# Performance work log

Hardware: AMD Instinct MI355X
Metric: run time of the kernel (lower is better)

The kernel has to match this reference:

```python
import jax, jax.numpy as jnp
import numpy as np

N = 50000      # nodes
E = 800000     # edges (before self loops)
IN_DIM = 256
HID = 64       # per-head hidden dim
HEADS = 4
NEG_SLOPE = 0.2


def setup_inputs() -> dict:
    key = jax.random.key(0)
    k1, k2, k3, k4, k5, k6 = jax.random.split(key, 6)
    x = jax.random.normal(k1, (N, IN_DIM), dtype=jnp.float32)
    edge_index = jax.random.randint(k2, (2, E), 0, N, dtype=jnp.int64)
    # GATConv params (PyG layout): lin weight, att_src, att_dst, bias
    W = jax.random.normal(k3, (IN_DIM, HEADS * HID), dtype=jnp.float32) / np.sqrt(IN_DIM)
    att_src = jax.random.normal(k4, (HEADS, HID), dtype=jnp.float32) / np.sqrt(HID)
    att_dst = jax.random.normal(k5, (HEADS, HID), dtype=jnp.float32) / np.sqrt(HID)
    bias = jnp.zeros((HEADS * HID,), dtype=jnp.float32)
    return {"x": x, "edge_index": edge_index, "W": W,
            "att_src": att_src, "att_dst": att_dst, "bias": bias}


def _gat_forward(x, edge_index, W, att_src, att_dst, bias):
    n = x.shape[0]
    # linear projection per head: [N, H, F]
    h = (x @ W).reshape(n, HEADS, HID)
    # per-node attention logits (computed once on nodes, then gathered)
    a_src = jnp.einsum('nhf,hf->nh', h, att_src)  # [N, H]
    a_dst = jnp.einsum('nhf,hf->nh', h, att_dst)  # [N, H]
    # add self loops (PyG default add_self_loops=True)
    loop = jnp.arange(n, dtype=edge_index.dtype)
    src = jnp.concatenate([edge_index[0], loop])  # [E+N]
    dst = jnp.concatenate([edge_index[1], loop])  # [E+N]
    # edge attention logits with LeakyReLU
    e = jax.nn.leaky_relu(a_src[src] + a_dst[dst], NEG_SLOPE)  # [E+N, H]
    # segment softmax over incoming edges of each destination node
    m = jax.ops.segment_max(e, dst, num_segments=n)            # [N, H]
    num = jnp.exp(e - m[dst])                                  # [E+N, H]
    denom = jax.ops.segment_sum(num, dst, num_segments=n)      # [N, H]
    alpha = num / denom[dst]                                   # [E+N, H]
    # scatter-aggregate weighted source features
    msg = alpha[:, :, None] * h[src]                           # [E+N, H, F]
    out = jax.ops.segment_sum(msg, dst, num_segments=n)        # [N, H, F]
    out = out.reshape(n, HEADS * HID) + bias
    # GraphEncoder.forward: ReLU then Dropout (dropout=0 -> identity)
    return jax.nn.relu(out)


def reference(x, edge_index, W, att_src, att_dst, bias):
    return _gat_forward(x, edge_index, W, att_src, att_dst, bias)
```

## Files before the change

kernel.cpp:

```cpp
#include <hip/hip_runtime.h>
#include <hip/hip_bf16.h>

#define N_NODES 50000
#define N_EDGES 800000
#define TOT_EDGES (N_EDGES + N_NODES)
#define IN_DIM 256
#define OUT_DIM 256
#define HEADS 4
#define NEG_SLOPE 0.2f
#define CAP 96

#define GBLK 782
#define LDS_STRIDE 264

typedef __bf16 bf16x8 __attribute__((ext_vector_type(8)));
typedef __bf16 bf16x4 __attribute__((ext_vector_type(4)));
typedef float f32x4 __attribute__((ext_vector_type(4)));

__device__ __forceinline__ float b2f(unsigned short u) {
    union { float f; unsigned int i; } v; v.i = ((unsigned int)u) << 16; return v.f;
}

__device__ __forceinline__ bool detect64(const int* __restrict__ ei, int t) {
    int nz = 0;
    for (int i = t; i < 1024; i += 256)
        if (ei[2 * i + 1] != 0) nz++;
    return __syncthreads_count(nz) == 0;
}

struct Args {
    const float* x; const int* ei; const float* W;
    const float* att_s; const float* att_d; const float* bias;
    float* out;
    __bf16* Wt; __bf16* h; float* a_src; float* a_dst;
    int* counts; int* ell;
};

__global__ void k_wt(Args A) {
    int k = blockIdx.x;
    int n = threadIdx.x;
    A.Wt[(size_t)n * IN_DIM + k] = (__bf16)A.W[(size_t)k * OUT_DIM + n];
}

__global__ __launch_bounds__(256) void k_fill(Args A) {
    bool is64 = detect64(A.ei, threadIdx.x);
    int i = blockIdx.x * 256 + threadIdx.x;
    const long long* ei64 = (const long long*)A.ei;
    if (i < N_EDGES) {
        int s, d;
        if (is64) { s = (int)ei64[i]; d = (int)ei64[N_EDGES + i]; }
        else      { s = A.ei[i];      d = A.ei[N_EDGES + i]; }
        int pos = atomicAdd(&A.counts[d], 1);
        if (pos < CAP) A.ell[(size_t)d * CAP + pos] = s;
    } else if (i < TOT_EDGES) {
        int n = i - N_EDGES;
        int pos = atomicAdd(&A.counts[n], 1);
        if (pos < CAP) A.ell[(size_t)n * CAP + pos] = n;
    }
}

__global__ __launch_bounds__(256) void k_gemm(Args A) {
    __shared__ __bf16 xs[64 * LDS_STRIDE];
    const int t = threadIdx.x;
    const int mbase = blockIdx.x * 64;
    const float4* __restrict__ x4 = (const float4*)A.x;
    const __bf16* __restrict__ Wt = A.Wt;

#pragma unroll
    for (int i = 0; i < 16; ++i) {
        int f = i * 256 + t;
        int row = f >> 6;
        int c4  = f & 63;
        int grow = mbase + row;
        if (grow >= N_NODES) grow = N_NODES - 1;
        float4 v = x4[(size_t)grow * 64 + c4];
        bf16x4 o = { (__bf16)v.x, (__bf16)v.y, (__bf16)v.z, (__bf16)v.w };
        *(bf16x4*)&xs[row * LDS_STRIDE + c4 * 4] = o;
    }
    __syncthreads();

    const int wave = t >> 6;
    const int lane = t & 63;
    const int cc   = lane & 15;
    const int quad = lane >> 4;
    const int n0   = wave * 64;
    f32x4 acc[4][4];
#pragma unroll
    for (int mt = 0; mt < 4; ++mt)
#pragma unroll
        for (int j = 0; j < 4; ++j) acc[mt][j] = (f32x4){0.f, 0.f, 0.f, 0.f};

    for (int k0 = 0; k0 < IN_DIM; k0 += 32) {
        bf16x8 b0 = *(const bf16x8*)(Wt + (size_t)(n0 + cc)      * IN_DIM + k0 + quad * 8);
        bf16x8 b1 = *(const bf16x8*)(Wt + (size_t)(n0 + 16 + cc) * IN_DIM + k0 + quad * 8);
        bf16x8 b2 = *(const bf16x8*)(Wt + (size_t)(n0 + 32 + cc) * IN_DIM + k0 + quad * 8);
        bf16x8 b3 = *(const bf16x8*)(Wt + (size_t)(n0 + 48 + cc) * IN_DIM + k0 + quad * 8);
#pragma unroll
        for (int mt = 0; mt < 4; ++mt) {
            bf16x8 a = *(const bf16x8*)&xs[(mt * 16 + cc) * LDS_STRIDE + k0 + quad * 8];
            acc[mt][0] = __builtin_amdgcn_mfma_f32_16x16x32_bf16(a, b0, acc[mt][0], 0, 0, 0);
            acc[mt][1] = __builtin_amdgcn_mfma_f32_16x16x32_bf16(a, b1, acc[mt][1], 0, 0, 0);
            acc[mt][2] = __builtin_amdgcn_mfma_f32_16x16x32_bf16(a, b2, acc[mt][2], 0, 0, 0);
            acc[mt][3] = __builtin_amdgcn_mfma_f32_16x16x32_bf16(a, b3, acc[mt][3], 0, 0, 0);
        }
    }

    float as0 = A.att_s[n0 + cc],      as1 = A.att_s[n0 + 16 + cc];
    float as2 = A.att_s[n0 + 32 + cc], as3 = A.att_s[n0 + 48 + cc];
    float ad0 = A.att_d[n0 + cc],      ad1 = A.att_d[n0 + 16 + cc];
    float ad2 = A.att_d[n0 + 32 + cc], ad3 = A.att_d[n0 + 48 + cc];
#pragma unroll
    for (int mt = 0; mt < 4; ++mt) {
#pragma unroll
        for (int r = 0; r < 4; ++r) {
            int row = mbase + mt * 16 + quad * 4 + r;
            float pS = acc[mt][0][r] * as0 + acc[mt][1][r] * as1
                     + acc[mt][2][r] * as2 + acc[mt][3][r] * as3;
            float pD = acc[mt][0][r] * ad0 + acc[mt][1][r] * ad1
                     + acc[mt][2][r] * ad2 + acc[mt][3][r] * ad3;
#pragma unroll
            for (int o = 8; o >= 1; o >>= 1) {
                pS += __shfl_xor(pS, o, 64);
                pD += __shfl_xor(pD, o, 64);
            }
            if (row < N_NODES && cc == 0) {
                A.a_src[row * 4 + wave] = pS;
                A.a_dst[row * 4 + wave] = pD;
            }
        }
    }

    __syncthreads();
#pragma unroll
    for (int mt = 0; mt < 4; ++mt)
#pragma unroll
        for (int j = 0; j < 4; ++j)
#pragma unroll
            for (int r = 0; r < 4; ++r)
                xs[(mt * 16 + quad * 4 + r) * LDS_STRIDE + n0 + j * 16 + cc] =
                    (__bf16)acc[mt][j][r];
    __syncthreads();
#pragma unroll
    for (int i = 0; i < 8; ++i) {
        int idx = i * 256 + t;
        int row = idx >> 5;
        int c8  = idx & 31;
        int grow = mbase + row;
        if (grow < N_NODES)
            *(bf16x8*)(A.h + (size_t)grow * OUT_DIM + c8 * 8) =
                *(const bf16x8*)&xs[row * LDS_STRIDE + c8 * 8];
    }
}

__global__ __launch_bounds__(256) void k_agg(Args A) {
    __shared__ float lds_all[4][CAP][4];
    int wave = threadIdx.x >> 6, lane = threadIdx.x & 63;
    int node = blockIdx.x * 4 + wave;
    if (node >= N_NODES) return;
    float (*lds)[4] = lds_all[wave];

    int base = node * CAP;
    int deg  = A.counts[node];
    if (deg > CAP) deg = CAP;
    const float4* as4 = (const float4*)A.a_src;
    float4 ad = ((const float4*)A.a_dst)[node];

    float4 smv = {0.f, 0.f, 0.f, 0.f};
    for (int e = lane; e < deg; e += 64) {
        int s = A.ell[base + e];
        float4 av = as4[s];
        float4 l;
        l.x = av.x + ad.x; l.x = l.x > 0.f ? l.x : NEG_SLOPE * l.x;
        l.y = av.y + ad.y; l.y = l.y > 0.f ? l.y : NEG_SLOPE * l.y;
        l.z = av.z + ad.z; l.z = l.z > 0.f ? l.z : NEG_SLOPE * l.z;
        l.w = av.w + ad.w; l.w = l.w > 0.f ? l.w : NEG_SLOPE * l.w;
        float4 e4;
        e4.x = __expf(l.x); e4.y = __expf(l.y);
        e4.z = __expf(l.z); e4.w = __expf(l.w);
        smv.x += e4.x; smv.y += e4.y; smv.z += e4.z; smv.w += e4.w;
        lds[e][0] = e4.x; lds[e][1] = e4.y; lds[e][2] = e4.z; lds[e][3] = e4.w;
    }
    int padEnd = (deg + 3) & ~3;
    for (int e = deg + lane; e < padEnd; e += 64) {
        lds[e][0] = 0.f; lds[e][1] = 0.f; lds[e][2] = 0.f; lds[e][3] = 0.f;
    }
#pragma unroll
    for (int o = 32; o >= 1; o >>= 1) {
        smv.x += __shfl_xor(smv.x, o, 64);
        smv.y += __shfl_xor(smv.y, o, 64);
        smv.z += __shfl_xor(smv.z, o, 64);
        smv.w += __shfl_xor(smv.w, o, 64);
    }

    int head = lane >> 4;
    float smh = head == 0 ? smv.x : head == 1 ? smv.y : head == 2 ? smv.z : smv.w;
    float inv_d = 1.f / smh;

    float acc0 = 0.f, acc1 = 0.f, acc2 = 0.f, acc3 = 0.f;
    const unsigned short* hs = reinterpret_cast<const unsigned short*>(A.h);
    int rEnd = padEnd;
    for (int e = 0; e < rEnd; e += 4) {
        int s0 = A.ell[base + e];
        int s1 = A.ell[base + ((e + 1 < deg) ? e + 1 : 0)];
        int s2 = A.ell[base + ((e + 2 < deg) ? e + 2 : 0)];
        int s3 = A.ell[base + ((e + 3 < deg) ? e + 3 : 0)];
        float al0 = lds[e][head];
        float al1 = lds[e + 1][head];
        float al2 = lds[e + 2][head];
        float al3 = lds[e + 3][head];
        ushort4 h0 = *(const ushort4*)(hs + (size_t)s0 * OUT_DIM + lane * 4);
        ushort4 h1 = *(const ushort4*)(hs + (size_t)s1 * OUT_DIM + lane * 4);
        ushort4 h2 = *(const ushort4*)(hs + (size_t)s2 * OUT_DIM + lane * 4);
        ushort4 h3 = *(const ushort4*)(hs + (size_t)s3 * OUT_DIM + lane * 4);
        acc0 += al0 * b2f(h0.x) + al1 * b2f(h1.x) + al2 * b2f(h2.x) + al3 * b2f(h3.x);
        acc1 += al0 * b2f(h0.y) + al1 * b2f(h1.y) + al2 * b2f(h2.y) + al3 * b2f(h3.y);
        acc2 += al0 * b2f(h0.z) + al1 * b2f(h1.z) + al2 * b2f(h2.z) + al3 * b2f(h3.z);
        acc3 += al0 * b2f(h0.w) + al1 * b2f(h1.w) + al2 * b2f(h2.w) + al3 * b2f(h3.w);
    }

    float4 bv = ((const float4*)A.bias)[lane];
    f32x4 o4;
    float v0 = acc0 * inv_d + bv.x;
    float v1 = acc1 * inv_d + bv.y;
    float v2 = acc2 * inv_d + bv.z;
    float v3 = acc3 * inv_d + bv.w;
    o4[0] = v0 > 0.f ? v0 : 0.f;
    o4[1] = v1 > 0.f ? v1 : 0.f;
    o4[2] = v2 > 0.f ? v2 : 0.f;
    o4[3] = v3 > 0.f ? v3 : 0.f;
    __builtin_nontemporal_store(o4, (f32x4*)A.out + (size_t)node * 64 + lane);
}

extern "C" void kernel_launch(void* const* d_in, const int* in_sizes, int n_in,
                              void* d_out, int out_size, void* d_ws, size_t ws_size,
                              hipStream_t stream) {
    (void)out_size; (void)ws_size;
    const void* p_x = nullptr; const void* p_ei = nullptr; const void* p_W = nullptr;
    const void* p_small[3] = {nullptr, nullptr, nullptr}; int nsmall = 0;
    for (int i = 0; i < n_in; ++i) {
        switch (in_sizes[i]) {
            case N_NODES * IN_DIM:      p_x = d_in[i]; break;
            case 2 * N_EDGES:           p_ei = d_in[i]; break;
            case IN_DIM * OUT_DIM:      p_W = d_in[i]; break;
            case OUT_DIM:               if (nsmall < 3) p_small[nsmall++] = d_in[i]; break;
            default: break;
        }
    }
    if (!p_x)  p_x  = d_in[0];
    if (!p_ei) p_ei = d_in[1];
    if (!p_W)  p_W  = d_in[2];
    if (nsmall < 3) { p_small[0] = d_in[3]; p_small[1] = d_in[4]; p_small[2] = d_in[5]; }

    char* ws = (char*)d_ws;
    size_t off = 0;
    auto alloc = [&](size_t bytes) -> void* {
        void* p = ws + off;
        off = (off + bytes + 255) & ~(size_t)255;
        return p;
    };
    Args A;
    A.Wt      = (__bf16*)alloc((size_t)IN_DIM * OUT_DIM * 2);
    A.h       = (__bf16*)alloc((size_t)N_NODES * OUT_DIM * 2);
    A.a_src   = (float*)alloc((size_t)N_NODES * HEADS * 4);
    A.a_dst   = (float*)alloc((size_t)N_NODES * HEADS * 4);
    A.counts  = (int*)alloc((size_t)N_NODES * 4);
    A.ell     = (int*)alloc((size_t)N_NODES * CAP * 4);

    A.x     = (const float*)p_x;
    A.ei    = (const int*)p_ei;
    A.W     = (const float*)p_W;
    A.att_s = (const float*)p_small[0];
    A.att_d = (const float*)p_small[1];
    A.bias  = (const float*)p_small[2];
    A.out   = (float*)d_out;

    hipMemsetAsync(A.counts, 0, (size_t)N_NODES * 4, stream);
    k_wt<<<dim3(IN_DIM), dim3(OUT_DIM), 0, stream>>>(A);
    k_fill<<<dim3((TOT_EDGES + 255) / 256), dim3(256), 0, stream>>>(A);
    k_gemm<<<dim3(GBLK), dim3(256), 0, stream>>>(A);
    k_agg<<<dim3((N_NODES + 3) / 4), dim3(256), 0, stream>>>(A);
}
```

Before: 263.3 us.

## Split aggregation per head with head-major h and fuse fill into GEMM launch

Stores the projected features h in head-major layout and launches aggregation with one block per (head, node group). Each pass then gathers only that head's 64-wide feature slice, a smaller working set meant to stay resident in cache during the random gathers. The edge-bucketing fill now runs as extra blocks inside the GEMM launch, and the counts memset is folded into the weight-transpose kernel, which cuts launches and lets fill and GEMM run side by side. The cost is that edge lists and attention logits are read once per head instead of once per node, and each lane issues narrower loads.

```diff
diff --git a/kernel.cpp b/kernel.cpp
--- a/kernel.cpp
+++ b/kernel.cpp
@@ -10,7 +10,9 @@
 #define NEG_SLOPE 0.2f
 #define CAP 96
 
+#define FBLK 512
 #define GBLK 782
+#define NBN  12500
 #define LDS_STRIDE 264
 
 typedef __bf16 bf16x8 __attribute__((ext_vector_type(8)));
@@ -32,7 +34,8 @@
     const float* x; const int* ei; const float* W;
     const float* att_s; const float* att_d; const float* bias;
     float* out;
-    __bf16* Wt; __bf16* h; float* a_src; float* a_dst;
+    __bf16* Wt; __bf16* h;
+    float* a_src; float* a_dst;
     int* counts; int* ell;
 };
 
@@ -40,195 +43,181 @@
     int k = blockIdx.x;
     int n = threadIdx.x;
     A.Wt[(size_t)n * IN_DIM + k] = (__bf16)A.W[(size_t)k * OUT_DIM + n];
-}
-
-__global__ __launch_bounds__(256) void k_fill(Args A) {
-    bool is64 = detect64(A.ei, threadIdx.x);
-    int i = blockIdx.x * 256 + threadIdx.x;
-    const long long* ei64 = (const long long*)A.ei;
-    if (i < N_EDGES) {
-        int s, d;
-        if (is64) { s = (int)ei64[i]; d = (int)ei64[N_EDGES + i]; }
-        else      { s = A.ei[i];      d = A.ei[N_EDGES + i]; }
-        int pos = atomicAdd(&A.counts[d], 1);
-        if (pos < CAP) A.ell[(size_t)d * CAP + pos] = s;
-    } else if (i < TOT_EDGES) {
-        int n = i - N_EDGES;
-        int pos = atomicAdd(&A.counts[n], 1);
-        if (pos < CAP) A.ell[(size_t)n * CAP + pos] = n;
-    }
-}
-
-__global__ __launch_bounds__(256) void k_gemm(Args A) {
+    int idx = blockIdx.x * 256 + threadIdx.x;
+    if (idx < N_NODES) A.counts[idx] = 0;
+}
+
+__global__ __launch_bounds__(256) void k_gemm_fill(Args A) {
     __shared__ __bf16 xs[64 * LDS_STRIDE];
     const int t = threadIdx.x;
-    const int mbase = blockIdx.x * 64;
-    const float4* __restrict__ x4 = (const float4*)A.x;
-    const __bf16* __restrict__ Wt = A.Wt;
-
-#pragma unroll
-    for (int i = 0; i < 16; ++i) {
-        int f = i * 256 + t;
-        int row = f >> 6;
-        int c4  = f & 63;
-        int grow = mbase + row;
-        if (grow >= N_NODES) grow = N_NODES - 1;
-        float4 v = x4[(size_t)grow * 64 + c4];
-        bf16x4 o = { (__bf16)v.x, (__bf16)v.y, (__bf16)v.z, (__bf16)v.w };
-        *(bf16x4*)&xs[row * LDS_STRIDE + c4 * 4] = o;
-    }
-    __syncthreads();
-
-    const int wave = t >> 6;
-    const int lane = t & 63;
-    const int cc   = lane & 15;
-    const int quad = lane >> 4;
-    const int n0   = wave * 64;
-    f32x4 acc[4][4];
-#pragma unroll
-    for (int mt = 0; mt < 4; ++mt)
-#pragma unroll
-        for (int j = 0; j < 4; ++j) acc[mt][j] = (f32x4){0.f, 0.f, 0.f, 0.f};
-
-    for (int k0 = 0; k0 < IN_DIM; k0 += 32) {
-        bf16x8 b0 = *(const bf16x8*)(Wt + (size_t)(n0 + cc)      * IN_DIM + k0 + quad * 8);
-        bf16x8 b1 = *(const bf16x8*)(Wt + (size_t)(n0 + 16 + cc) * IN_DIM + k0 + quad * 8);
-        bf16x8 b2 = *(const bf16x8*)(Wt + (size_t)(n0 + 32 + cc) * IN_DIM + k0 + quad * 8);
-        bf16x8 b3 = *(const bf16x8*)(Wt + (size_t)(n0 + 48 + cc) * IN_DIM + k0 + quad * 8);
+
+    if (blockIdx.x >= FBLK) {
+        const int mbase = (blockIdx.x - FBLK) * 64;
+        const float4* __restrict__ x4 = (const float4*)A.x;
+        const __bf16* __restrict__ Wt = A.Wt;
+
+#pragma unroll
+        for (int i = 0; i < 16; ++i) {
+            int f = i * 256 + t;
+            int row = f >> 6;
+            int c4  = f & 63;
+            int grow = mbase + row;
+            if (grow >= N_NODES) grow = N_NODES - 1;
+            float4 v = x4[(size_t)grow * 64 + c4];
+            bf16x4 o = { (__bf16)v.x, (__bf16)v.y, (__bf16)v.z, (__bf16)v.w };
+            *(bf16x4*)&xs[row * LDS_STRIDE + c4 * 4] = o;
+        }
+        __syncthreads();
+
+        const int wave = t >> 6;
+        const int lane = t & 63;
+        const int cc   = lane & 15;
+        const int quad = lane >> 4;
+        const int n0   = wave * 64;
+        f32x4 acc[4][4];
+#pragma unroll
+        for (int mt = 0; mt < 4; ++mt)
+#pragma unroll
+            for (int j = 0; j < 4; ++j) acc[mt][j] = (f32x4){0.f, 0.f, 0.f, 0.f};
+
+        for (int k0 = 0; k0 < IN_DIM; k0 += 32) {
+            bf16x8 b0 = *(const bf16x8*)(Wt + (size_t)(n0 + cc)      * IN_DIM + k0 + quad * 8);
+            bf16x8 b1 = *(const bf16x8*)(Wt + (size_t)(n0 + 16 + cc) * IN_DIM + k0 + quad * 8);
+            bf16x8 b2 = *(const bf16x8*)(Wt + (size_t)(n0 + 32 + cc) * IN_DIM + k0 + quad * 8);
+            bf16x8 b3 = *(const bf16x8*)(Wt + (size_t)(n0 + 48 + cc) * IN_DIM + k0 + quad * 8);
+#pragma unroll
+            for (int mt = 0; mt < 4; ++mt) {
+                bf16x8 a = *(const bf16x8*)&xs[(mt * 16 + cc) * LDS_STRIDE + k0 + quad * 8];
+                acc[mt][0] = __builtin_amdgcn_mfma_f32_16x16x32_bf16(a, b0, acc[mt][0], 0, 0, 0);
+                acc[mt][1] = __builtin_amdgcn_mfma_f32_16x16x32_bf16(a, b1, acc[mt][1], 0, 0, 0);
+                acc[mt][2] = __builtin_amdgcn_mfma_f32_16x16x32_bf16(a, b2, acc[mt][2], 0, 0, 0);
+                acc[mt][3] = __builtin_amdgcn_mfma_f32_16x16x32_bf16(a, b3, acc[mt][3], 0, 0, 0);
+            }
+        }
+
+        float as0 = A.att_s[n0 + cc],      as1 = A.att_s[n0 + 16 + cc];
+        float as2 = A.att_s[n0 + 32 + cc], as3 = A.att_s[n0 + 48 + cc];
+        float ad0 = A.att_d[n0 + cc],      ad1 = A.att_d[n0 + 16 + cc];
+        float ad2 = A.att_d[n0 + 32 + cc], ad3 = A.att_d[n0 + 48 + cc];
 #pragma unroll
         for (int mt = 0; mt < 4; ++mt) {
-            bf16x8 a = *(const bf16x8*)&xs[(mt * 16 + cc) * LDS_STRIDE + k0 + quad * 8];
-            acc[mt][0] = __builtin_amdgcn_mfma_f32_16x16x32_bf16(a, b0, acc[mt][0], 0, 0, 0);
-            acc[mt][1] = __builtin_amdgcn_mfma_f32_16x16x32_bf16(a, b1, acc[mt][1], 0, 0, 0);
-            acc[mt][2] = __builtin_amdgcn_mfma_f32_16x16x32_bf16(a, b2, acc[mt][2], 0, 0, 0);
-            acc[mt][3] = __builtin_amdgcn_mfma_f32_16x16x32_bf16(a, b3, acc[mt][3], 0, 0, 0);
-        }
-    }
-
-    float as0 = A.att_s[n0 + cc],      as1 = A.att_s[n0 + 16 + cc];
-    float as2 = A.att_s[n0 + 32 + cc], as3 = A.att_s[n0 + 48 + cc];
-    float ad0 = A.att_d[n0 + cc],      ad1 = A.att_d[n0 + 16 + cc];
-    float ad2 = A.att_d[n0 + 32 + cc], ad3 = A.att_d[n0 + 48 + cc];
-#pragma unroll
-    for (int mt = 0; mt < 4; ++mt) {
-#pragma unroll
-        for (int r = 0; r < 4; ++r) {
-            int row = mbase + mt * 16 + quad * 4 + r;
-            float pS = acc[mt][0][r] * as0 + acc[mt][1][r] * as1
-                     + acc[mt][2][r] * as2 + acc[mt][3][r] * as3;
-            float pD = acc[mt][0][r] * ad0 + acc[mt][1][r] * ad1
-                     + acc[mt][2][r] * ad2 + acc[mt][3][r] * ad3;
-#pragma unroll
-            for (int o = 8; o >= 1; o >>= 1) {
-                pS += __shfl_xor(pS, o, 64);
-                pD += __shfl_xor(pD, o, 64);
+#pragma unroll
+            for (int r = 0; r < 4; ++r) {
+                int row = mbase + mt * 16 + quad * 4 + r;
+                float pS = acc[mt][0][r] * as0 + acc[mt][1][r] * as1
+                         + acc[mt][2][r] * as2 + acc[mt][3][r] * as3;
+                float pD = acc[mt][0][r] * ad0 + acc[mt][1][r] * ad1
+                         + acc[mt][2][r] * ad2 + acc[mt][3][r] * ad3;
+#pragma unroll
+                for (int o = 8; o >= 1; o >>= 1) {
+                    pS += __shfl_xor(pS, o, 64);
+                    pD += __shfl_xor(pD, o, 64);
+                }
+                if (row < N_NODES && cc == 0) {
+                    A.a_src[row * 4 + wave] = pS;
+                    A.a_dst[row * 4 + wave] = pD;
+                }
             }
-            if (row < N_NODES && cc == 0) {
-                A.a_src[row * 4 + wave] = pS;
-                A.a_dst[row * 4 + wave] = pD;
+        }
+
+        __syncthreads();
+#pragma unroll
+        for (int mt = 0; mt < 4; ++mt)
+#pragma unroll
+            for (int j = 0; j < 4; ++j)
+#pragma unroll
+                for (int r = 0; r < 4; ++r)
+                    xs[(mt * 16 + quad * 4 + r) * LDS_STRIDE + n0 + j * 16 + cc] =
+                        (__bf16)acc[mt][j][r];
+        __syncthreads();
+#pragma unroll
+        for (int i = 0; i < 8; ++i) {
+            int idx = i * 256 + t;
+            int row = idx >> 5;
+            int c8  = idx & 31;
+            int hd  = c8 >> 3, d8 = c8 & 7;
+            int grow = mbase + row;
+            if (grow < N_NODES)
+                *(bf16x8*)(A.h + ((size_t)hd * N_NODES + grow) * 64 + d8 * 8) =
+                    *(const bf16x8*)&xs[row * LDS_STRIDE + c8 * 8];
+        }
+    } else {
+        bool is64 = detect64(A.ei, t);
+        const long long* ei64 = (const long long*)A.ei;
+        for (int i = blockIdx.x * 256 + t; i < TOT_EDGES; i += FBLK * 256) {
+            int s, d;
+            if (i < N_EDGES) {
+                if (is64) { s = (int)ei64[i]; d = (int)ei64[N_EDGES + i]; }
+                else      { s = A.ei[i];      d = A.ei[N_EDGES + i]; }
+            } else {
+                s = d = i - N_EDGES;
             }
-        }
-    }
-
-    __syncthreads();
-#pragma unroll
-    for (int mt = 0; mt < 4; ++mt)
-#pragma unroll
-        for (int j = 0; j < 4; ++j)
-#pragma unroll
-            for (int r = 0; r < 4; ++r)
-                xs[(mt * 16 + quad * 4 + r) * LDS_STRIDE + n0 + j * 16 + cc] =
-                    (__bf16)acc[mt][j][r];
-    __syncthreads();
-#pragma unroll
-    for (int i = 0; i < 8; ++i) {
-        int idx = i * 256 + t;
-        int row = idx >> 5;
-        int c8  = idx & 31;
-        int grow = mbase + row;
-        if (grow < N_NODES)
-            *(bf16x8*)(A.h + (size_t)grow * OUT_DIM + c8 * 8) =
-                *(const bf16x8*)&xs[row * LDS_STRIDE + c8 * 8];
+            int pos = atomicAdd(&A.counts[d], 1);
+            if (pos < CAP) A.ell[(size_t)d * CAP + pos] = s;
+        }
     }
 }
 
 __global__ __launch_bounds__(256) void k_agg(Args A) {
-    __shared__ float lds_all[4][CAP][4];
-    int wave = threadIdx.x >> 6, lane = threadIdx.x & 63;
-    int node = blockIdx.x * 4 + wave;
+    __shared__ float alp_all[4][CAP];
+    const int wave = threadIdx.x >> 6, lane = threadIdx.x & 63;
+    const int head = blockIdx.x / NBN;
+    const int nb   = blockIdx.x % NBN;
+    const int node = nb * 4 + wave;
     if (node >= N_NODES) return;
-    float (*lds)[4] = lds_all[wave];
-
-    int base = node * CAP;
-    int deg  = A.counts[node];
+    float* alp = alp_all[wave];
+
+    const int base = node * CAP;
+    int deg = A.counts[node];
     if (deg > CAP) deg = CAP;
-    const float4* as4 = (const float4*)A.a_src;
-    float4 ad = ((const float4*)A.a_dst)[node];
-
-    float4 smv = {0.f, 0.f, 0.f, 0.f};
+    const float adh = A.a_dst[node * 4 + head];
+
+    float sm = 0.f;
     for (int e = lane; e < deg; e += 64) {
         int s = A.ell[base + e];
-        float4 av = as4[s];
-        float4 l;
-        l.x = av.x + ad.x; l.x = l.x > 0.f ? l.x : NEG_SLOPE * l.x;
-        l.y = av.y + ad.y; l.y = l.y > 0.f ? l.y : NEG_SLOPE * l.y;
-        l.z = av.z + ad.z; l.z = l.z > 0.f ? l.z : NEG_SLOPE * l.z;
-        l.w = av.w + ad.w; l.w = l.w > 0.f ? l.w : NEG_SLOPE * l.w;
-        float4 e4;
-        e4.x = __expf(l.x); e4.y = __expf(l.y);
-        e4.z = __expf(l.z); e4.w = __expf(l.w);
-        smv.x += e4.x; smv.y += e4.y; smv.z += e4.z; smv.w += e4.w;
-        lds[e][0] = e4.x; lds[e][1] = e4.y; lds[e][2] = e4.z; lds[e][3] = e4.w;
+        float l = A.a_src[s * 4 + head] + adh;
+        l = l > 0.f ? l : NEG_SLOPE * l;
+        float al = __expf(l);
+        sm += al;
+        alp[e] = al;
     }
     int padEnd = (deg + 3) & ~3;
-    for (int e = deg + lane; e < padEnd; e += 64) {
-        lds[e][0] = 0.f; lds[e][1] = 0.f; lds[e][2] = 0.f; lds[e][3] = 0.f;
-    }
-#pragma unroll
-    for (int o = 32; o >= 1; o >>= 1) {
-        smv.x += __shfl_xor(smv.x, o, 64);
-        smv.y += __shfl_xor(smv.y, o, 64);
-        smv.z += __shfl_xor(smv.z, o, 64);
-        smv.w += __shfl_xor(smv.w, o, 64);
-    }
-
-    int head = lane >> 4;
-    float smh = head == 0 ? smv.x : head == 1 ? smv.y : head == 2 ? smv.z : smv.w;
-    float inv_d = 1.f / smh;
-
-    float acc0 = 0.f, acc1 = 0.f, acc2 = 0.f, acc3 = 0.f;
-    const unsigned short* hs = reinterpret_cast<const unsigned short*>(A.h);
-    int rEnd = padEnd;
-    for (int e = 0; e < rEnd; e += 4) {
-        int s0 = A.ell[base + e];
-        int s1 = A.ell[base + ((e + 1 < deg) ? e + 1 : 0)];
-        int s2 = A.ell[base + ((e + 2 < deg) ? e + 2 : 0)];
-        int s3 = A.ell[base + ((e + 3 < deg) ? e + 3 : 0)];
-        float al0 = lds[e][head];
-        float al1 = lds[e + 1][head];
-        float al2 = lds[e + 2][head];
-        float al3 = lds[e + 3][head];
-        ushort4 h0 = *(const ushort4*)(hs + (size_t)s0 * OUT_DIM + lane * 4);
-        ushort4 h1 = *(const ushort4*)(hs + (size_t)s1 * OUT_DIM + lane * 4);
-        ushort4 h2 = *(const ushort4*)(hs + (size_t)s2 * OUT_DIM + lane * 4);
-        ushort4 h3 = *(const ushort4*)(hs + (size_t)s3 * OUT_DIM + lane * 4);
-        acc0 += al0 * b2f(h0.x) + al1 * b2f(h1.x) + al2 * b2f(h2.x) + al3 * b2f(h3.x);
-        acc1 += al0 * b2f(h0.y) + al1 * b2f(h1.y) + al2 * b2f(h2.y) + al3 * b2f(h3.y);
-        acc2 += al0 * b2f(h0.z) + al1 * b2f(h1.z) + al2 * b2f(h2.z) + al3 * b2f(h3.z);
-        acc3 += al0 * b2f(h0.w) + al1 * b2f(h1.w) + al2 * b2f(h2.w) + al3 * b2f(h3.w);
-    }
-
-    float4 bv = ((const float4*)A.bias)[lane];
-    f32x4 o4;
-    float v0 = acc0 * inv_d + bv.x;
-    float v1 = acc1 * inv_d + bv.y;
-    float v2 = acc2 * inv_d + bv.z;
-    float v3 = acc3 * inv_d + bv.w;
-    o4[0] = v0 > 0.f ? v0 : 0.f;
-    o4[1] = v1 > 0.f ? v1 : 0.f;
-    o4[2] = v2 > 0.f ? v2 : 0.f;
-    o4[3] = v3 > 0.f ? v3 : 0.f;
-    __builtin_nontemporal_store(o4, (f32x4*)A.out + (size_t)node * 64 + lane);
+    for (int e = deg + lane; e < padEnd; e += 64) alp[e] = 0.f;
+#pragma unroll
+    for (int o = 32; o >= 1; o >>= 1) sm += __shfl_xor(sm, o, 64);
+    const float inv_d = 1.f / sm;
+
+    const int grp = lane >> 4, d16 = lane & 15;
+    const unsigned short* __restrict__ hH =
+        (const unsigned short*)A.h + (size_t)head * N_NODES * 64;
+    float a0 = 0.f, a1 = 0.f, a2 = 0.f, a3 = 0.f;
+    for (int e0 = 0; e0 < padEnd; e0 += 4) {
+        int e = e0 + grp;
+        int s = (e < deg) ? A.ell[base + e] : 0;
+        float al = alp[e];
+        ushort4 hv = *(const ushort4*)(hH + (size_t)s * 64 + d16 * 4);
+        a0 += al * b2f(hv.x); a1 += al * b2f(hv.y);
+        a2 += al * b2f(hv.z); a3 += al * b2f(hv.w);
+    }
+#pragma unroll
+    for (int o = 32; o >= 16; o >>= 1) {
+        a0 += __shfl_xor(a0, o, 64); a1 += __shfl_xor(a1, o, 64);
+        a2 += __shfl_xor(a2, o, 64); a3 += __shfl_xor(a3, o, 64);
+    }
+    if (grp == 0) {
+        float4 bv = *(const float4*)(A.bias + head * 64 + d16 * 4);
+        float v0 = a0 * inv_d + bv.x;
+        float v1 = a1 * inv_d + bv.y;
+        float v2 = a2 * inv_d + bv.z;
+        float v3 = a3 * inv_d + bv.w;
+        f32x4 o4;
+        o4[0] = v0 > 0.f ? v0 : 0.f;
+        o4[1] = v1 > 0.f ? v1 : 0.f;
+        o4[2] = v2 > 0.f ? v2 : 0.f;
+        o4[3] = v3 > 0.f ? v3 : 0.f;
+        __builtin_nontemporal_store(o4,
+            (f32x4*)(A.out + (size_t)node * OUT_DIM + head * 64) + d16);
+    }
 }
 
 extern "C" void kernel_launch(void* const* d_in, const int* in_sizes, int n_in,
@@ -274,9 +263,7 @@
     A.bias  = (const float*)p_small[2];
     A.out   = (float*)d_out;
 
-    hipMemsetAsync(A.counts, 0, (size_t)N_NODES * 4, stream);
     k_wt<<<dim3(IN_DIM), dim3(OUT_DIM), 0, stream>>>(A);
-    k_fill<<<dim3((TOT_EDGES + 255) / 256), dim3(256), 0, stream>>>(A);
-    k_gemm<<<dim3(GBLK), dim3(256), 0, stream>>>(A);
-    k_agg<<<dim3((N_NODES + 3) / 4), dim3(256), 0, stream>>>(A);
-}
+    k_gemm_fill<<<dim3(FBLK + GBLK), dim3(256), 0, stream>>>(A);
+    k_agg<<<dim3(HEADS * NBN), dim3(256), 0, stream>>>(A);
+}
```

New measurement: 331.0 us. +25.7%, slower.
